# Optimization experiments

Hardware: AMD Instinct MI355X
Metric: run time of the kernel (lower is better)

## Reference

```python
import jax, jax.numpy as jnp
import numpy as np
import math

NX = 1024
N_HEAD = 16
HEAD_DIM = NX // N_HEAD
N_CTX = 2048
REL_VOCAB = 64
B = 2
S = 2048


def setup_inputs() -> dict:
    key = jax.random.key(0)
    ks = jax.random.split(key, 7)
    x = jax.random.normal(ks[0], (B, S, NX), dtype=jnp.float32)
    rel = jax.random.randint(ks[1], (B, S, S), 0, REL_VOCAB, dtype=jnp.int64)
    sc = 0.02
    Wqkv = jax.random.normal(ks[2], (NX, 3 * NX), dtype=jnp.float32) * sc
    bqkv = jnp.zeros((3 * NX,), dtype=jnp.float32)
    Wproj = jax.random.normal(ks[3], (NX, NX), dtype=jnp.float32) * sc
    bproj = jnp.zeros((NX,), dtype=jnp.float32)
    rel_emb = jax.random.normal(ks[4], (REL_VOCAB, N_HEAD), dtype=jnp.float32) * sc
    return {"x": x, "Wqkv": Wqkv, "bqkv": bqkv, "Wproj": Wproj,
            "bproj": bproj, "rel_emb": rel_emb, "rel": rel}


def reference(x, Wqkv, bqkv, Wproj, bproj, rel_emb, rel):
    Bsz, Sq, _ = x.shape
    qkv = x @ Wqkv + bqkv                      # [B,S,3*nx]
    q, k, v = jnp.split(qkv, 3, axis=-1)
    def split_heads(t):                        # [B,S,nx] -> [B,H,S,D]
        return t.reshape(Bsz, Sq, N_HEAD, HEAD_DIM).transpose(0, 2, 1, 3)
    q, k, v = split_heads(q), split_heads(k), split_heads(v)
    w = jnp.einsum('bhqd,bhkd->bhqk', q, k) / math.sqrt(HEAD_DIM)
    bmask = jnp.tril(jnp.ones((Sq, Sq), dtype=w.dtype))[None, None]  # [1,1,S,S]
    w = w * bmask - 1e10 * (1.0 - bmask)
    relw = rel_emb[rel].transpose(0, 3, 1, 2)  # [B,S,S,H] -> [B,H,S,S]
    w = w * (relw * bmask)                     # faithful: masked scores become 0
    p = jax.nn.softmax(w, axis=-1)
    a = jnp.einsum('bhqk,bhkd->bhqd', p, v)
    a = a.transpose(0, 2, 1, 3).reshape(Bsz, Sq, NX)  # merge heads
    return a @ Wproj + bproj
```

## Files before the change

kernel.cpp:

```cpp
#include <hip/hip_runtime.h>

typedef unsigned short u16;
typedef unsigned char u8;
typedef __attribute__((ext_vector_type(8))) short short8;
typedef __attribute__((ext_vector_type(4))) short short4v;
typedef __attribute__((ext_vector_type(4))) float f32x4;

#define GLD16(g, l) __builtin_amdgcn_global_load_lds( \
    (const __attribute__((address_space(1))) void*)(g), \
    (__attribute__((address_space(3))) void*)(l), 16, 0, 0)

__device__ __forceinline__ float bf2f(u16 u){
  union { unsigned int i; float f; } v; v.i = ((unsigned int)u) << 16; return v.f;
}
__device__ __forceinline__ u16 f2bf(float f){
  union { float f; unsigned int i; } v; v.f = f;
  unsigned int u = v.i;
  unsigned int r = (u + 0x7FFFu + ((u >> 16) & 1u)) >> 16;
  return (u16)r;
}

__device__ __forceinline__ f32x4 mfma16(short4v a, short4v b, f32x4 c){
#if __has_builtin(__builtin_amdgcn_mfma_f32_16x16x16bf16_1k)
  return __builtin_amdgcn_mfma_f32_16x16x16bf16_1k(a, b, c, 0, 0, 0);
#else
  asm volatile("s_nop 1\n\tv_mfma_f32_16x16x16_bf16 %0, %1, %2, %0" : "+v"(c) : "v"(a), "v"(b));
  return c;
#endif
}

__global__ void cvt_k(const float* __restrict__ x, u16* __restrict__ o, int n4){
  int i = blockIdx.x * 256 + threadIdx.x;
  if (i >= n4) return;
  float4 v = ((const float4*)x)[i];
  unsigned long long pk = (unsigned long long)f2bf(v.x)
    | ((unsigned long long)f2bf(v.y) << 16)
    | ((unsigned long long)f2bf(v.z) << 32)
    | ((unsigned long long)f2bf(v.w) << 48);
  ((unsigned long long*)o)[i] = pk;
}

__global__ void rel8_k(const int* __restrict__ r, u8* __restrict__ o, int n4){
  int i = blockIdx.x * 256 + threadIdx.x;
  if (i >= n4) return;
  int4 v = ((const int4*)r)[i];
  unsigned int pk = (unsigned int)(v.x & 255) | ((unsigned int)(v.y & 255) << 8)
    | ((unsigned int)(v.z & 255) << 16) | ((unsigned int)(v.w & 255) << 24);
  ((unsigned int*)o)[i] = pk;
}

__global__ void tconv_k(const float* __restrict__ W, u16* __restrict__ Wt, int K, int N){
  __shared__ float tl[32][33];
  int n0 = blockIdx.x * 32, k0 = blockIdx.y * 32;
  for (int i = threadIdx.y; i < 32; i += 8)
    tl[i][threadIdx.x] = W[(size_t)(k0 + i) * N + n0 + threadIdx.x];
  __syncthreads();
  for (int i = threadIdx.y; i < 32; i += 8)
    Wt[(size_t)(n0 + i) * K + k0 + threadIdx.x] = f2bf(tl[threadIdx.x][i]);
}

template<int MODE>
__global__ __launch_bounds__(256) void gemm_bt_k(const u16* __restrict__ A, const u16* __restrict__ Bt,
                                                 const float* __restrict__ bias,
                                                 u16* __restrict__ oq, u16* __restrict__ okk, u16* __restrict__ ov,
                                                 float* __restrict__ of,
                                                 int M, int N, int K){
  __shared__ u16 la[128 * 32];
  __shared__ u16 lb[128 * 32];
  const int t = threadIdx.x, w = t >> 6, lane = t & 63;
  const int l15 = lane & 15, l4 = lane >> 4;
  const int m0 = blockIdx.y * 128, n0 = blockIdx.x * 128;
  const int wr = w >> 1, wc = w & 1;
  f32x4 acc[4][4] = {};
  const u16* Abase = A + (size_t)m0 * K;
  const u16* Bbase = Bt + (size_t)n0 * K;
  for (int kt = 0; kt < K; kt += 32){
    __syncthreads();
#pragma unroll
    for (int i = 0; i < 2; ++i){
      int chunk = i * 256 + t;
      int row = chunk >> 2, cg = chunk & 3;
      GLD16(Abase + (size_t)row * K + kt + cg * 8, &la[(i * 256 + w * 64) * 8]);
    }
#pragma unroll
    for (int i = 0; i < 2; ++i){
      int chunk = i * 256 + t;
      int row = chunk >> 2, cg = chunk & 3;
      GLD16(Bbase + (size_t)row * K + kt + cg * 8, &lb[(i * 256 + w * 64) * 8]);
    }
    asm volatile("s_waitcnt vmcnt(0)" ::: "memory");
    __syncthreads();
    short8 af[4], bfr[4];
#pragma unroll
    for (int mi = 0; mi < 4; ++mi)
      af[mi] = *(const short8*)&la[(wr * 64 + mi * 16 + l15) * 32 + l4 * 8];
#pragma unroll
    for (int ni = 0; ni < 4; ++ni)
      bfr[ni] = *(const short8*)&lb[(wc * 64 + ni * 16 + l15) * 32 + l4 * 8];
#pragma unroll
    for (int mi = 0; mi < 4; ++mi)
#pragma unroll
      for (int ni = 0; ni < 4; ++ni)
        acc[mi][ni] = __builtin_amdgcn_mfma_f32_16x16x32_bf16(af[mi], bfr[ni], acc[mi][ni], 0, 0, 0);
  }
#pragma unroll
  for (int mi = 0; mi < 4; ++mi){
#pragma unroll
    for (int ni = 0; ni < 4; ++ni){
#pragma unroll
      for (int r = 0; r < 4; ++r){
        int m = m0 + wr * 64 + mi * 16 + l4 * 4 + r;
        int n = n0 + wc * 64 + ni * 16 + l15;
        float v = acc[mi][ni][r] + bias[n];
        if (MODE == 0){
          int tt = n >> 10, rr = n & 1023, head = rr >> 6, d = rr & 63;
          int b = m >> 11, s = m & 2047;
          u16* dst = (tt == 0) ? oq : (tt == 1) ? okk : ov;
          dst[(((size_t)(b * 16 + head)) * 2048 + s) * 64 + d] = f2bf(v);
        } else {
          of[(size_t)m * N + n] = v;
        }
      }
    }
  }
}

__global__ __launch_bounds__(256) void transpose_v_k(const u16* __restrict__ vb, u16* __restrict__ vt,
                                                     float* __restrict__ vpart){
  __shared__ u16 tl[64][65];
  int bh = blockIdx.x >> 5, c = blockIdx.x & 31, s0 = c * 64;
  int t = threadIdx.x;
#pragma unroll
  for (int rsub = 0; rsub < 16; ++rsub){
    int idx = rsub * 256 + t;
    int i = idx >> 6, d = idx & 63;
    tl[i][d] = vb[(((size_t)bh * 2048) + s0 + i) * 64 + d];
  }
  __syncthreads();
#pragma unroll
  for (int rsub = 0; rsub < 16; ++rsub){
    int idx = rsub * 256 + t;
    int d = idx >> 6, j = idx & 63;
    int pj = (j & 3) | (((j >> 2) & 3) << 4) | (((j >> 4) & 3) << 2);
    vt[(((size_t)bh * 64) + d) * 2048 + s0 + pj] = tl[j][d];
  }
  if (t < 64){
    float s = 0.f;
#pragma unroll 8
    for (int j = 0; j < 64; ++j) s += bf2f(tl[j][t]);
    vpart[((size_t)bh * 32 + c) * 64 + t] = s;
  }
}

__global__ void vsufscan_k(const float* __restrict__ vpart, float* __restrict__ vsuf){
  int bh = blockIdx.x, d = threadIdx.x;
  float run = 0.f;
  vsuf[((size_t)bh * 33 + 32) * 64 + d] = 0.f;
  for (int c = 31; c >= 0; --c){
    run += vpart[((size_t)bh * 32 + c) * 64 + d];
    vsuf[((size_t)bh * 33 + c) * 64 + d] = run;
  }
}

template<int U8>
__global__ __launch_bounds__(256, 2) void attn_k(const u16* __restrict__ qb, const u16* __restrict__ kb,
                                                 const u16* __restrict__ vt, const float* __restrict__ vsuf,
                                                 const void* __restrict__ relp, const float* __restrict__ rel_emb,
                                                 u16* __restrict__ ab){
  __shared__ u16 Kt[2][64 * 64];
  __shared__ u16 Vt[2][64 * 64];
  __shared__ float remb[64];
  const int qp = blockIdx.x, bh = blockIdx.y;
  const int b = bh >> 4, h = bh & 15;
  const int TA = qp, TB = 31 - qp;
  const int q0A = TA * 64, q0B = TB * 64;
  const int tid = threadIdx.x, w = tid >> 6, lane = tid & 63;
  const int l15 = lane & 15, l4 = lane >> 4;
  if (tid < 64) remb[tid] = rel_emb[tid * 16 + h] * (0.125f * 1.44269504088896f);
  const u16* kbh = kb + ((size_t)bh * 2048) * 64;
  const u16* vbh = vt + ((size_t)bh * 64) * 2048;
  const u16* qA = qb + (((size_t)bh * 2048) + q0A + w * 16 + l15) * 64 + l4 * 8;
  const u16* qB = qb + (((size_t)bh * 2048) + q0B + w * 16 + l15) * 64 + l4 * 8;
  const short8 aqA0 = *(const short8*)qA, aqA1 = *(const short8*)(qA + 32);
  const short8 aqB0 = *(const short8*)qB, aqB1 = *(const short8*)(qB + 32);
  const u8*  r8A  = (const u8*)relp + ((size_t)b * 2048 + q0A + w * 16 + l15) * 2048;
  const u8*  r8B  = (const u8*)relp + ((size_t)b * 2048 + q0B + w * 16 + l15) * 2048;
  const int* r32A = (const int*)relp + ((size_t)b * 2048 + q0A + w * 16 + l15) * 2048;
  const int* r32B = (const int*)relp + ((size_t)b * 2048 + q0B + w * 16 + l15) * 2048;

  const int srow0 = (tid >> 3), srow1 = 32 + (tid >> 3);
  const int scs = tid & 7;
  const int sc0 = scs ^ (srow0 & 7), sc1 = scs ^ (srow1 & 7);
  const int sldsoff = (w * 64) * 8;

#define STAGE(ktile, buf) do {                                                       \
    GLD16(kbh + (size_t)((ktile) * 64 + srow0) * 64 + sc0 * 8, &Kt[buf][sldsoff]);   \
    GLD16(kbh + (size_t)((ktile) * 64 + srow1) * 64 + sc1 * 8, &Kt[buf][2048 + sldsoff]); \
    GLD16(vbh + (size_t)srow0 * 2048 + (ktile) * 64 + sc0 * 8, &Vt[buf][sldsoff]);   \
    GLD16(vbh + (size_t)srow1 * 2048 + (ktile) * 64 + sc1 * 8, &Vt[buf][2048 + sldsoff]); \
  } while (0)

  f32x4 acc[4] = {};
  float rsum = 0.f;
  unsigned int relc[4], reln[4];

  auto relload = [&](bool isA, int kt, unsigned int* dst){
    int off = kt * 64 + 4 * l4;
    if (U8){
      const u8* p = isA ? r8A : r8B;
#pragma unroll
      for (int t = 0; t < 4; ++t) dst[t] = *(const unsigned int*)(p + off + 16 * t);
    } else {
      const int* p = isA ? r32A : r32B;
#pragma unroll
      for (int t = 0; t < 4; ++t){
        int4 v4 = *(const int4*)(p + off + 16 * t);
        dst[t] = (unsigned int)(v4.x & 255) | ((unsigned int)(v4.y & 255) << 8)
               | ((unsigned int)(v4.z & 255) << 16) | ((unsigned int)(v4.w & 255) << 24);
      }
    }
  };

  auto writeout = [&](int Td, int q0){
    asm volatile("s_nop 7\n\ts_nop 7" :::);
    float s = rsum;
    s += __shfl_xor(s, 16);
    s += __shfl_xor(s, 32);
    float invZ = 1.f / (s + (float)(2048 - (Td + 1) * 64));
    int qg = q0 + w * 16 + l15;
    const float* sufp = vsuf + ((size_t)bh * 33 + Td + 1) * 64;
#pragma unroll
    for (int ni = 0; ni < 4; ++ni){
      float4 sv = *(const float4*)(sufp + ni * 16 + 4 * l4);
      unsigned int lo = (unsigned int)f2bf((acc[ni][0] + sv.x) * invZ)
                      | ((unsigned int)f2bf((acc[ni][1] + sv.y) * invZ) << 16);
      unsigned int hi = (unsigned int)f2bf((acc[ni][2] + sv.z) * invZ)
                      | ((unsigned int)f2bf((acc[ni][3] + sv.w) * invZ) << 16);
      uint2 o; o.x = lo; o.y = hi;
      *(uint2*)(ab + ((size_t)b * 2048 + qg) * 1024 + h * 64 + ni * 16 + 4 * l4) = o;
    }
  };

  STAGE(0, 0);
  relload(true, 0, relc);
  __syncthreads();

  const int TOT = TA + TB + 2;
  for (int it = 0; it < TOT; ++it){
    const bool isA = (it <= TA);
    const int kt = isA ? it : (it - TA - 1);
    const int cur = it & 1;
    const int Tlim = isA ? TA : TB;

    if (it + 1 < TOT){
      const bool nIsA = (it + 1 <= TA);
      const int nkt = nIsA ? (it + 1) : (it - TA);
      STAGE(nkt, cur ^ 1);
      relload(nIsA, nkt, reln);
    }

    const short8 a0 = isA ? aqA0 : aqB0;
    const short8 a1 = isA ? aqA1 : aqB1;
    const bool diag = (kt == Tlim);

    short4v pk[4];
    __builtin_amdgcn_s_setprio(1);
#pragma unroll
    for (int t = 0; t < 4; ++t){
      const int krow = 16 * t + l15;
      const u16* kbase = &Kt[cur][krow * 64];
      short8 bk0 = *(const short8*)&kbase[((l4)     ^ (krow & 7)) * 8];
      short8 bk1 = *(const short8*)&kbase[((4 + l4) ^ (krow & 7)) * 8];
      f32x4 sf = {0.f, 0.f, 0.f, 0.f};
      sf = __builtin_amdgcn_mfma_f32_16x16x32_bf16(bk0, a0, sf, 0, 0, 0);
      sf = __builtin_amdgcn_mfma_f32_16x16x32_bf16(bk1, a1, sf, 0, 0, 0);
      unsigned int rw = relc[t];
      const int kk = 16 * t + 4 * l4;
#pragma unroll
      for (int r = 0; r < 4; ++r){
        float sc = sf[r] * remb[(rw >> (8 * r)) & 255];
        if (diag) sc = (kk + r <= w * 16 + l15) ? sc : 0.f;
        float p = __builtin_amdgcn_exp2f(sc);
        rsum += p;
        pk[t][r] = (short)f2bf(p);
      }
    }
    asm volatile("s_nop 2" :::);
#pragma unroll
    for (int ni = 0; ni < 4; ++ni){
      const int drow = ni * 16 + l15;
      const u16* vbase = &Vt[cur][drow * 64];
      short8 vv0 = *(const short8*)&vbase[(((2 * l4)     ^ (drow & 7))) * 8];
      short8 vv1 = *(const short8*)&vbase[(((2 * l4 + 1) ^ (drow & 7))) * 8];
      short4v va0 = {vv0[0], vv0[1], vv0[2], vv0[3]};
      short4v va1 = {vv0[4], vv0[5], vv0[6], vv0[7]};
      short4v va2 = {vv1[0], vv1[1], vv1[2], vv1[3]};
      short4v va3 = {vv1[4], vv1[5], vv1[6], vv1[7]};
      acc[ni] = mfma16(va0, pk[0], acc[ni]);
      acc[ni] = mfma16(va1, pk[1], acc[ni]);
      acc[ni] = mfma16(va2, pk[2], acc[ni]);
      acc[ni] = mfma16(va3, pk[3], acc[ni]);
    }
    __builtin_amdgcn_s_setprio(0);

    if (isA && it == TA){
      writeout(TA, q0A);
#pragma unroll
      for (int ni = 0; ni < 4; ++ni) acc[ni] = f32x4{0.f, 0.f, 0.f, 0.f};
      rsum = 0.f;
    }
#pragma unroll
    for (int t = 0; t < 4; ++t) relc[t] = reln[t];
    __syncthreads();
  }
#undef STAGE
  writeout(TB, q0B);
}

extern "C" void kernel_launch(void* const* d_in, const int* in_sizes, int n_in,
                              void* d_out, int out_size, void* d_ws, size_t ws_size,
                              hipStream_t stream){
  const float* x       = (const float*)d_in[0];
  const float* Wqkv    = (const float*)d_in[1];
  const float* bqkv    = (const float*)d_in[2];
  const float* Wproj   = (const float*)d_in[3];
  const float* bproj   = (const float*)d_in[4];
  const float* rel_emb = (const float*)d_in[5];
  const int*   rel     = (const int*)d_in[6];
  float* out = (float*)d_out;

  char* ws = (char*)d_ws;
  u16* xb     = (u16*)(ws);
  u16* wqkvT  = (u16*)(ws + (8ull  << 20));
  u16* wprojT = (u16*)(ws + (14ull << 20));
  u16* qb     = (u16*)(ws + (16ull << 20));
  u16* kb     = (u16*)(ws + (24ull << 20));
  u16* vb     = (u16*)(ws + (32ull << 20));
  u16* vtb    = (u16*)(ws + (40ull << 20));
  float* vsuf = (float*)(ws + (48ull << 20));
  float* vpart= (float*)(ws + (48ull << 20) + (512ull << 10));
  u8*   rel8  = (u8*)(ws + (49ull << 20));
  const bool useU8 = ws_size >= (58ull << 20);

  cvt_k<<<4096, 256, 0, stream>>>(x, xb, 1048576);
  tconv_k<<<dim3(96, 32), dim3(32, 8), 0, stream>>>(Wqkv, wqkvT, 1024, 3072);
  tconv_k<<<dim3(32, 32), dim3(32, 8), 0, stream>>>(Wproj, wprojT, 1024, 1024);
  if (useU8) rel8_k<<<8192, 256, 0, stream>>>(rel, rel8, 2097152);
  gemm_bt_k<0><<<dim3(24, 32), 256, 0, stream>>>(xb, wqkvT, bqkv, qb, kb, vb, nullptr, 4096, 3072, 1024);
  transpose_v_k<<<1024, 256, 0, stream>>>(vb, vtb, vpart);
  vsufscan_k<<<32, 64, 0, stream>>>(vpart, vsuf);
  if (useU8)
    attn_k<1><<<dim3(16, 32), 256, 0, stream>>>(qb, kb, vtb, vsuf, rel8, rel_emb, xb);
  else
    attn_k<0><<<dim3(16, 32), 256, 0, stream>>>(qb, kb, vtb, vsuf, rel, rel_emb, xb);
  gemm_bt_k<1><<<dim3(8, 32), 256, 0, stream>>>(xb, wprojT, bproj, nullptr, nullptr, nullptr, out, 4096, 1024, 1024);
}
```

Baseline: 172.8 us.

## Split attention key range across two wave groups and deepen GEMM K-tiles

The attention kernel now runs 512 threads per block: two groups of four waves each handle half of the 33 key tiles for the paired query blocks. Partial accumulators and row sums are merged through LDS scratch before writeout. This doubles parallelism per block to hide latency. Separately, the GEMM now stages 64-wide K tiles with XOR-swizzled LDS to reduce bank conflicts and barrier count, and the projection GEMM uses 64-wide N tiles to launch more blocks. The costs are higher LDS and register pressure and an extra cross-group reduction.

```diff
diff --git a/kernel.cpp b/kernel.cpp
--- a/kernel.cpp
+++ b/kernel.cpp
@@ -59,58 +59,71 @@
     Wt[(size_t)(n0 + i) * K + k0 + threadIdx.x] = f2bf(tl[threadIdx.x][i]);
 }
 
-template<int MODE>
+template<int BN, int MODE>
 __global__ __launch_bounds__(256) void gemm_bt_k(const u16* __restrict__ A, const u16* __restrict__ Bt,
                                                  const float* __restrict__ bias,
                                                  u16* __restrict__ oq, u16* __restrict__ okk, u16* __restrict__ ov,
                                                  float* __restrict__ of,
                                                  int M, int N, int K){
-  __shared__ u16 la[128 * 32];
-  __shared__ u16 lb[128 * 32];
+  __shared__ u16 la[128 * 64];
+  __shared__ u16 lb[BN * 64];
   const int t = threadIdx.x, w = t >> 6, lane = t & 63;
   const int l15 = lane & 15, l4 = lane >> 4;
-  const int m0 = blockIdx.y * 128, n0 = blockIdx.x * 128;
+  const int m0 = blockIdx.y * 128, n0 = blockIdx.x * BN;
   const int wr = w >> 1, wc = w & 1;
-  f32x4 acc[4][4] = {};
+  constexpr int NI = BN / 32;
+  f32x4 acc[4][NI] = {};
   const u16* Abase = A + (size_t)m0 * K;
   const u16* Bbase = Bt + (size_t)n0 * K;
-  for (int kt = 0; kt < K; kt += 32){
+  for (int kt = 0; kt < K; kt += 64){
     __syncthreads();
 #pragma unroll
-    for (int i = 0; i < 2; ++i){
+    for (int i = 0; i < 4; ++i){
       int chunk = i * 256 + t;
-      int row = chunk >> 2, cg = chunk & 3;
-      GLD16(Abase + (size_t)row * K + kt + cg * 8, &la[(i * 256 + w * 64) * 8]);
-    }
-#pragma unroll
-    for (int i = 0; i < 2; ++i){
+      int row = chunk >> 3, cs = chunk & 7;
+      int c = cs ^ (row & 7);
+      GLD16(Abase + (size_t)row * K + kt + c * 8, &la[(i * 256 + w * 64) * 8]);
+    }
+#pragma unroll
+    for (int i = 0; i < BN / 32; ++i){
       int chunk = i * 256 + t;
-      int row = chunk >> 2, cg = chunk & 3;
-      GLD16(Bbase + (size_t)row * K + kt + cg * 8, &lb[(i * 256 + w * 64) * 8]);
+      int row = chunk >> 3, cs = chunk & 7;
+      int c = cs ^ (row & 7);
+      GLD16(Bbase + (size_t)row * K + kt + c * 8, &lb[(i * 256 + w * 64) * 8]);
     }
     asm volatile("s_waitcnt vmcnt(0)" ::: "memory");
     __syncthreads();
-    short8 af[4], bfr[4];
+    short8 af[4][2], bfr[NI][2];
+#pragma unroll
+    for (int mi = 0; mi < 4; ++mi){
+      int row = wr * 64 + mi * 16 + l15;
+#pragma unroll
+      for (int h = 0; h < 2; ++h)
+        af[mi][h] = *(const short8*)&la[row * 64 + (((h * 4 + l4) ^ (row & 7)) * 8)];
+    }
+#pragma unroll
+    for (int ni = 0; ni < NI; ++ni){
+      int row = wc * (BN / 2) + ni * 16 + l15;
+#pragma unroll
+      for (int h = 0; h < 2; ++h)
+        bfr[ni][h] = *(const short8*)&lb[row * 64 + (((h * 4 + l4) ^ (row & 7)) * 8)];
+    }
 #pragma unroll
     for (int mi = 0; mi < 4; ++mi)
-      af[mi] = *(const short8*)&la[(wr * 64 + mi * 16 + l15) * 32 + l4 * 8];
-#pragma unroll
-    for (int ni = 0; ni < 4; ++ni)
-      bfr[ni] = *(const short8*)&lb[(wc * 64 + ni * 16 + l15) * 32 + l4 * 8];
-#pragma unroll
-    for (int mi = 0; mi < 4; ++mi)
-#pragma unroll
-      for (int ni = 0; ni < 4; ++ni)
-        acc[mi][ni] = __builtin_amdgcn_mfma_f32_16x16x32_bf16(af[mi], bfr[ni], acc[mi][ni], 0, 0, 0);
+#pragma unroll
+      for (int ni = 0; ni < NI; ++ni){
+        acc[mi][ni] = __builtin_amdgcn_mfma_f32_16x16x32_bf16(af[mi][0], bfr[ni][0], acc[mi][ni], 0, 0, 0);
+        acc[mi][ni] = __builtin_amdgcn_mfma_f32_16x16x32_bf16(af[mi][1], bfr[ni][1], acc[mi][ni], 0, 0, 0);
+      }
   }
 #pragma unroll
   for (int mi = 0; mi < 4; ++mi){
 #pragma unroll
-    for (int ni = 0; ni < 4; ++ni){
+    for (int ni = 0; ni < NI; ++ni){
 #pragma unroll
       for (int r = 0; r < 4; ++r){
         int m = m0 + wr * 64 + mi * 16 + l4 * 4 + r;
-        int n = n0 + wc * 64 + ni * 16 + l15;
+        int n = n0 + wc * (BN / 2) + ni * 16 + l15;
         float v = acc[mi][ni][r] + bias[n];
         if (MODE == 0){
           int tt = n >> 10, rr = n & 1023, head = rr >> 6, d = rr & 63;
@@ -163,19 +176,22 @@
 }
 
 template<int U8>
-__global__ __launch_bounds__(256, 2) void attn_k(const u16* __restrict__ qb, const u16* __restrict__ kb,
+__global__ __launch_bounds__(512, 4) void attn_k(const u16* __restrict__ qb, const u16* __restrict__ kb,
                                                  const u16* __restrict__ vt, const float* __restrict__ vsuf,
                                                  const void* __restrict__ relp, const float* __restrict__ rel_emb,
                                                  u16* __restrict__ ab){
-  __shared__ u16 Kt[2][64 * 64];
-  __shared__ u16 Vt[2][64 * 64];
+  __shared__ u16 Kt[2][2][64 * 64];
+  __shared__ u16 Vt[2][2][64 * 64];
   __shared__ float remb[64];
+  __shared__ float scrsum[4][64];
   const int qp = blockIdx.x, bh = blockIdx.y;
   const int b = bh >> 4, h = bh & 15;
   const int TA = qp, TB = 31 - qp;
   const int q0A = TA * 64, q0B = TB * 64;
-  const int tid = threadIdx.x, w = tid >> 6, lane = tid & 63;
+  const int tid = threadIdx.x;
+  const int wv = tid >> 6, g = wv >> 2, w = wv & 3, lane = tid & 63;
   const int l15 = lane & 15, l4 = lane >> 4;
+  const int tg = tid & 255;
   if (tid < 64) remb[tid] = rel_emb[tid * 16 + h] * (0.125f * 1.44269504088896f);
   const u16* kbh = kb + ((size_t)bh * 2048) * 64;
   const u16* vbh = vt + ((size_t)bh * 64) * 2048;
@@ -188,20 +204,21 @@
   const int* r32A = (const int*)relp + ((size_t)b * 2048 + q0A + w * 16 + l15) * 2048;
   const int* r32B = (const int*)relp + ((size_t)b * 2048 + q0B + w * 16 + l15) * 2048;
 
-  const int srow0 = (tid >> 3), srow1 = 32 + (tid >> 3);
-  const int scs = tid & 7;
+  const int srow0 = (tg >> 3), srow1 = 32 + (tg >> 3);
+  const int scs = tg & 7;
   const int sc0 = scs ^ (srow0 & 7), sc1 = scs ^ (srow1 & 7);
   const int sldsoff = (w * 64) * 8;
 
-#define STAGE(ktile, buf) do {                                                       \
-    GLD16(kbh + (size_t)((ktile) * 64 + srow0) * 64 + sc0 * 8, &Kt[buf][sldsoff]);   \
-    GLD16(kbh + (size_t)((ktile) * 64 + srow1) * 64 + sc1 * 8, &Kt[buf][2048 + sldsoff]); \
-    GLD16(vbh + (size_t)srow0 * 2048 + (ktile) * 64 + sc0 * 8, &Vt[buf][sldsoff]);   \
-    GLD16(vbh + (size_t)srow1 * 2048 + (ktile) * 64 + sc1 * 8, &Vt[buf][2048 + sldsoff]); \
+#define STAGE(ktile, buf) do {                                                          \
+    GLD16(kbh + (size_t)((ktile) * 64 + srow0) * 64 + sc0 * 8, &Kt[g][buf][sldsoff]);   \
+    GLD16(kbh + (size_t)((ktile) * 64 + srow1) * 64 + sc1 * 8, &Kt[g][buf][2048 + sldsoff]); \
+    GLD16(vbh + (size_t)srow0 * 2048 + (ktile) * 64 + sc0 * 8, &Vt[g][buf][sldsoff]);   \
+    GLD16(vbh + (size_t)srow1 * 2048 + (ktile) * 64 + sc1 * 8, &Vt[g][buf][2048 + sldsoff]); \
   } while (0)
 
   f32x4 acc[4] = {};
-  float rsum = 0.f;
+  f32x4 accS[4] = {};
+  float rsum = 0.f, rsumS = 0.f;
   unsigned int relc[4], reln[4];
 
   auto relload = [&](bool isA, int kt, unsigned int* dst){
@@ -241,34 +258,39 @@
     }
   };
 
-  STAGE(0, 0);
-  relload(true, 0, relc);
+  const int lo = g ? 17 : 0;
+  const int hi = g ? 33 : 17;
+
+  {
+    bool isA0 = (lo <= TA);
+    int kt0 = isA0 ? lo : lo - TA - 1;
+    STAGE(kt0, 0);
+    relload(isA0, kt0, relc);
+  }
   __syncthreads();
 
-  const int TOT = TA + TB + 2;
-  for (int it = 0; it < TOT; ++it){
+  for (int it = lo; it < hi; ++it){
     const bool isA = (it <= TA);
     const int kt = isA ? it : (it - TA - 1);
-    const int cur = it & 1;
-    const int Tlim = isA ? TA : TB;
-
-    if (it + 1 < TOT){
-      const bool nIsA = (it + 1 <= TA);
-      const int nkt = nIsA ? (it + 1) : (it - TA);
+    const int cur = (it - lo) & 1;
+
+    if (it + 1 < hi){
+      const bool nA = (it + 1 <= TA);
+      const int nkt = nA ? (it + 1) : (it - TA);
       STAGE(nkt, cur ^ 1);
-      relload(nIsA, nkt, reln);
+      relload(nA, nkt, reln);
     }
 
     const short8 a0 = isA ? aqA0 : aqB0;
     const short8 a1 = isA ? aqA1 : aqB1;
-    const bool diag = (kt == Tlim);
+    const bool diag = (kt == (isA ? TA : TB));
 
     short4v pk[4];
     __builtin_amdgcn_s_setprio(1);
 #pragma unroll
     for (int t = 0; t < 4; ++t){
       const int krow = 16 * t + l15;
-      const u16* kbase = &Kt[cur][krow * 64];
+      const u16* kbase = &Kt[g][cur][krow * 64];
       short8 bk0 = *(const short8*)&kbase[((l4)     ^ (krow & 7)) * 8];
       short8 bk1 = *(const short8*)&kbase[((4 + l4) ^ (krow & 7)) * 8];
       f32x4 sf = {0.f, 0.f, 0.f, 0.f};
@@ -289,7 +311,7 @@
 #pragma unroll
     for (int ni = 0; ni < 4; ++ni){
       const int drow = ni * 16 + l15;
-      const u16* vbase = &Vt[cur][drow * 64];
+      const u16* vbase = &Vt[g][cur][drow * 64];
       short8 vv0 = *(const short8*)&vbase[(((2 * l4)     ^ (drow & 7))) * 8];
       short8 vv1 = *(const short8*)&vbase[(((2 * l4 + 1) ^ (drow & 7))) * 8];
       short4v va0 = {vv0[0], vv0[1], vv0[2], vv0[3]};
@@ -303,18 +325,50 @@
     }
     __builtin_amdgcn_s_setprio(0);
 
-    if (isA && it == TA){
-      writeout(TA, q0A);
+    if (it == TA){
+      if (g == 0){
+        writeout(TA, q0A);
+      } else {
+#pragma unroll
+        for (int ni = 0; ni < 4; ++ni) accS[ni] = acc[ni];
+        rsumS = rsum;
+      }
 #pragma unroll
       for (int ni = 0; ni < 4; ++ni) acc[ni] = f32x4{0.f, 0.f, 0.f, 0.f};
       rsum = 0.f;
     }
-#pragma unroll
-    for (int t = 0; t < 4; ++t) relc[t] = reln[t];
+    if (it + 1 < hi){
+#pragma unroll
+      for (int t = 0; t < 4; ++t) relc[t] = reln[t];
+    }
     __syncthreads();
   }
 #undef STAGE
-  writeout(TB, q0B);
+  if (g) __syncthreads();
+
+  const bool Ble = (TA <= 16);
+  if (!Ble && g == 1) writeout(TB, q0B);
+
+  float* scr = (float*)&Kt[0][0][0];
+  if (Ble ? (g == 0) : (g == 1)){
+#pragma unroll
+    for (int ni = 0; ni < 4; ++ni){
+      f32x4 src = Ble ? acc[ni] : accS[ni];
+      *(f32x4*)&scr[(w * 16 + l15) * 68 + ni * 16 + 4 * l4] = src;
+    }
+    scrsum[w][lane] = Ble ? rsum : rsumS;
+  }
+  __syncthreads();
+  if (Ble ? (g == 1) : (g == 0)){
+#pragma unroll
+    for (int ni = 0; ni < 4; ++ni){
+      f32x4 d = *(const f32x4*)&scr[(w * 16 + l15) * 68 + ni * 16 + 4 * l4];
+      acc[ni][0] += d[0]; acc[ni][1] += d[1]; acc[ni][2] += d[2]; acc[ni][3] += d[3];
+    }
+    rsum += scrsum[w][lane];
+    if (Ble) writeout(TB, q0B);
+    else     writeout(TA, q0A);
+  }
 }
 
 extern "C" void kernel_launch(void* const* d_in, const int* in_sizes, int n_in,
@@ -346,12 +400,12 @@
   tconv_k<<<dim3(96, 32), dim3(32, 8), 0, stream>>>(Wqkv, wqkvT, 1024, 3072);
   tconv_k<<<dim3(32, 32), dim3(32, 8), 0, stream>>>(Wproj, wprojT, 1024, 1024);
   if (useU8) rel8_k<<<8192, 256, 0, stream>>>(rel, rel8, 2097152);
-  gemm_bt_k<0><<<dim3(24, 32), 256, 0, stream>>>(xb, wqkvT, bqkv, qb, kb, vb, nullptr, 4096, 3072, 1024);
+  gemm_bt_k<128, 0><<<dim3(24, 32), 256, 0, stream>>>(xb, wqkvT, bqkv, qb, kb, vb, nullptr, 4096, 3072, 1024);
   transpose_v_k<<<1024, 256, 0, stream>>>(vb, vtb, vpart);
   vsufscan_k<<<32, 64, 0, stream>>>(vpart, vsuf);
   if (useU8)
-    attn_k<1><<<dim3(16, 32), 256, 0, stream>>>(qb, kb, vtb, vsuf, rel8, rel_emb, xb);
+    attn_k<1><<<dim3(16, 32), 512, 0, stream>>>(qb, kb, vtb, vsuf, rel8, rel_emb, xb);
   else
-    attn_k<0><<<dim3(16, 32), 256, 0, stream>>>(qb, kb, vtb, vsuf, rel, rel_emb, xb);
-  gemm_bt_k<1><<<dim3(8, 32), 256, 0, stream>>>(xb, wprojT, bproj, nullptr, nullptr, nullptr, out, 4096, 1024, 1024);
-}
+    attn_k<0><<<dim3(16, 32), 512, 0, stream>>>(qb, kb, vtb, vsuf, rel, rel_emb, xb);
+  gemm_bt_k<64, 1><<<dim3(16, 32), 256, 0, stream>>>(xb, wprojT, bproj, nullptr, nullptr, nullptr, out, 4096, 1024, 1024);
+}
```

Measured after the change: 191.2 us. +10.7%, slower.
